# Performance work log

Measured on AMD Instinct MI355X. Metric: run time of the kernel, lower is better.

The kernel has to match this reference:

```python
import jax, jax.numpy as jnp
import numpy as np

NEG_INF = -9e15


def setup_inputs() -> dict:
    key = jax.random.key(0)
    k1, k2, k3, k4, k5, k6 = jax.random.split(key, 6)
    B, N, F_IN, F_OUT = 16, 2048, 256, 128
    inputs = jax.random.normal(k1, (B, N, F_IN), dtype=jnp.float32)
    adj_matrix = jax.random.randint(k2, (B, N, N), 0, 2, dtype=jnp.int32)
    W = jax.random.normal(k3, (F_OUT, F_IN), dtype=jnp.float32) * (1.0 / np.sqrt(F_IN))
    b_W = jax.random.normal(k4, (F_OUT,), dtype=jnp.float32) * 0.02
    a = jax.random.normal(k5, (1, 2 * F_OUT), dtype=jnp.float32) * (1.0 / np.sqrt(2 * F_OUT))
    b_a = jax.random.normal(k6, (1,), dtype=jnp.float32) * 0.02
    return {"inputs": inputs, "adj_matrix": adj_matrix, "W": W, "b_W": b_W, "a": a, "b_a": b_a}


def reference(inputs, adj_matrix, W, b_W, a, b_a):
    # wh: [B, N, H]
    wh = jnp.einsum('bnf,hf->bnh', inputs, W) + b_W
    H = wh.shape[-1]
    # linear_self_W([wh_i, wh_j]) = a1.wh_i + a2.wh_j + b  (rank-1 linear over concat)
    a1 = a[0, :H]
    a2 = a[0, H:]
    src = jnp.einsum('bnh,h->bn', wh, a1)  # [B, N] contribution of row node i
    dst = jnp.einsum('bnh,h->bn', wh, a2)  # [B, N] contribution of col node j
    e = jax.nn.leaky_relu(src[:, :, None] + dst[:, None, :] + b_a[0], negative_slope=0.01)
    e = jnp.where(adj_matrix > 0, e, NEG_INF)
    att = jax.nn.softmax(e, axis=-1)  # dropout in eval mode = identity
    return jax.nn.elu(jnp.einsum('bij,bjh->bih', att, wh))
```

## Files before the change

kernel.cpp:

```cpp
#include <hip/hip_runtime.h>


#define BDIM 16
#define NDIM 2048
#define FIN 256
#define HDIM 128

typedef short short8 __attribute__((ext_vector_type(8)));
typedef float floatx4 __attribute__((ext_vector_type(4)));

__device__ __forceinline__ unsigned short f2bf(float x) {
    unsigned int u = __float_as_uint(x);
    unsigned int r = (u + 0x7fffu + ((u >> 16) & 1u)) >> 16;
    return (unsigned short)r;
}
__device__ __forceinline__ float bf2f(unsigned short s) {
    return __uint_as_float(((unsigned int)s) << 16);
}

__global__ __launch_bounds__(256) void k_wh(const float* __restrict__ X,
                                            const float* __restrict__ W,
                                            const float* __restrict__ bW,
                                            const float* __restrict__ a,
                                            float* __restrict__ src,
                                            float* __restrict__ dst,
                                            unsigned short* __restrict__ whF) {
    __shared__ short lds[27648];
    short (*ah)[72] = (short(*)[72])lds;
    short (*al)[72] = (short(*)[72])(lds + 4608);
    short (*bh)[72] = (short(*)[72])(lds + 9216);
    short (*bl)[72] = (short(*)[72])(lds + 18432);
    short (*tb)[72] = (short(*)[72])lds;

    const int tid = threadIdx.x;
    const long row0 = (long)blockIdx.x * 64;
    const int w = tid >> 6, lane = tid & 63;
    const int lm = lane & 15, q = lane >> 4;

    float a1v[8], a2v[8], bwv[8];
    #pragma unroll
    for (int nt = 0; nt < 8; nt++) {
        a1v[nt] = a[nt * 16 + lm];
        a2v[nt] = a[HDIM + nt * 16 + lm];
        bwv[nt] = bW[nt * 16 + lm];
    }

    floatx4 acc[8];
    #pragma unroll
    for (int nt = 0; nt < 8; nt++) acc[nt] = (floatx4){0.f, 0.f, 0.f, 0.f};

    for (int k0 = 0; k0 < FIN; k0 += 64) {
        #pragma unroll
        for (int u = 0; u < 4; u++) {
            int idx = tid + u * 256;
            int r = idx >> 4, fc = (idx & 15) * 4;
            float4 v = *reinterpret_cast<const float4*>(X + (row0 + r) * FIN + k0 + fc);
            union { unsigned short s[4]; uint2 u2; } ph, pl;
            ph.s[0] = f2bf(v.x); pl.s[0] = f2bf(v.x - bf2f(ph.s[0]));
            ph.s[1] = f2bf(v.y); pl.s[1] = f2bf(v.y - bf2f(ph.s[1]));
            ph.s[2] = f2bf(v.z); pl.s[2] = f2bf(v.z - bf2f(ph.s[2]));
            ph.s[3] = f2bf(v.w); pl.s[3] = f2bf(v.w - bf2f(ph.s[3]));
            *reinterpret_cast<uint2*>(&ah[r][fc]) = ph.u2;
            *reinterpret_cast<uint2*>(&al[r][fc]) = pl.u2;
        }
        #pragma unroll
        for (int u = 0; u < 8; u++) {
            int idx = tid + u * 256;
            int hh = idx >> 4, fc = (idx & 15) * 4;
            float4 v = *reinterpret_cast<const float4*>(W + hh * FIN + k0 + fc);
            union { unsigned short s[4]; uint2 u2; } ph, pl;
            ph.s[0] = f2bf(v.x); pl.s[0] = f2bf(v.x - bf2f(ph.s[0]));
            ph.s[1] = f2bf(v.y); pl.s[1] = f2bf(v.y - bf2f(ph.s[1]));
            ph.s[2] = f2bf(v.z); pl.s[2] = f2bf(v.z - bf2f(ph.s[2]));
            ph.s[3] = f2bf(v.w); pl.s[3] = f2bf(v.w - bf2f(ph.s[3]));
            *reinterpret_cast<uint2*>(&bh[hh][fc]) = ph.u2;
            *reinterpret_cast<uint2*>(&bl[hh][fc]) = pl.u2;
        }
        __syncthreads();
        #pragma unroll
        for (int ks = 0; ks < 64; ks += 32) {
            short8 afh = *reinterpret_cast<const short8*>(&ah[w * 16 + lm][ks + q * 8]);
            short8 afl = *reinterpret_cast<const short8*>(&al[w * 16 + lm][ks + q * 8]);
            #pragma unroll
            for (int nt = 0; nt < 8; nt++) {
                short8 bfh = *reinterpret_cast<const short8*>(&bh[nt * 16 + lm][ks + q * 8]);
                short8 bfl = *reinterpret_cast<const short8*>(&bl[nt * 16 + lm][ks + q * 8]);
                acc[nt] = __builtin_amdgcn_mfma_f32_16x16x32_bf16(afh, bfh, acc[nt], 0, 0, 0);
                acc[nt] = __builtin_amdgcn_mfma_f32_16x16x32_bf16(afh, bfl, acc[nt], 0, 0, 0);
                acc[nt] = __builtin_amdgcn_mfma_f32_16x16x32_bf16(afl, bfh, acc[nt], 0, 0, 0);
            }
        }
        __syncthreads();
    }

    float s1[4] = {0.f, 0.f, 0.f, 0.f}, s2[4] = {0.f, 0.f, 0.f, 0.f};
    #pragma unroll
    for (int nt = 0; nt < 8; nt++) {
        #pragma unroll
        for (int r = 0; r < 4; r++) {
            float v = acc[nt][r] + bwv[nt];
            s1[r] += v * a1v[nt];
            s2[r] += v * a2v[nt];
            tb[nt * 16 + lm][w * 16 + q * 4 + r] = f2bf(v);
        }
    }
    #pragma unroll
    for (int r = 0; r < 4; r++) {
        #pragma unroll
        for (int o = 1; o < 16; o <<= 1) {
            s1[r] += __shfl_xor(s1[r], o);
            s2[r] += __shfl_xor(s2[r], o);
        }
    }
    if (lm == 0) {
        #pragma unroll
        for (int r = 0; r < 4; r++) {
            long row = row0 + w * 16 + q * 4 + r;
            src[row] = s1[r];
            dst[row] = s2[r];
        }
    }
    __syncthreads();
    const int b = (int)(row0 >> 11);
    const int jc0 = (int)((row0 & 2047) >> 5);
    const int f = tid >> 4;
    const int sub = tid & 15;
    const int jcrel = f >> 3, ht = f & 7;
    const size_t fbase = (((size_t)b * 64 + jc0 + jcrel) * 8 + ht) * 512;
    #pragma unroll
    for (int i = 0; i < 4; i++) {
        int l = sub * 4 + i;
        uint4 v = *reinterpret_cast<const uint4*>(&tb[ht * 16 + (l & 15)][jcrel * 32 + (l >> 4) * 8]);
        *reinterpret_cast<uint4*>(whF + fbase + l * 8) = v;
    }
}

__global__ __launch_bounds__(256) void k_attn(const int* __restrict__ adj,
                                              const unsigned short* __restrict__ whF,
                                              const float* __restrict__ src,
                                              const float* __restrict__ dst,
                                              const float* __restrict__ ba_p,
                                              float* __restrict__ out) {
    __shared__ float lred[64];
    __shared__ float linv_s[64];

    const int tid = threadIdx.x;
    const int b = blockIdx.x >> 5;
    const int i0 = (blockIdx.x & 31) * 64;
    const int wave = tid >> 6, lane = tid & 63;
    const int lm = lane & 15, q = lane >> 4;
    const int irow = i0 + wave * 16 + lm;

    const float si = src[b * NDIM + irow] + ba_p[0];
    const int* adjp = adj + ((size_t)(b * NDIM + irow)) * NDIM + q * 8;
    const float* dstp = dst + b * NDIM + q * 8;
    const unsigned short* whFb = whF + (size_t)b * 64 * 8 * 512 + lane * 8;

    floatx4 acc[8];
    #pragma unroll
    for (int hj = 0; hj < 8; hj++) acc[hj] = (floatx4){0.f, 0.f, 0.f, 0.f};
    float lpart = 0.f;

    int4 m[2][2];
    float4 d[2][2];
    short8 bfr[2][8];
    m[0][0] = *reinterpret_cast<const int4*>(adjp);
    m[0][1] = *reinterpret_cast<const int4*>(adjp + 4);
    d[0][0] = *reinterpret_cast<const float4*>(dstp);
    d[0][1] = *reinterpret_cast<const float4*>(dstp + 4);
    #pragma unroll
    for (int hj = 0; hj < 8; hj++) bfr[0][hj] = *reinterpret_cast<const short8*>(whFb + hj * 512);

    #pragma unroll 2
    for (int t = 0; t < NDIM / 32; t++) {
        const int p = t & 1, pn = p ^ 1;
        if (t + 1 < NDIM / 32) {
            const int* ap = adjp + (t + 1) * 32;
            m[pn][0] = *reinterpret_cast<const int4*>(ap);
            m[pn][1] = *reinterpret_cast<const int4*>(ap + 4);
            const float* dp = dstp + (t + 1) * 32;
            d[pn][0] = *reinterpret_cast<const float4*>(dp);
            d[pn][1] = *reinterpret_cast<const float4*>(dp + 4);
            const unsigned short* wp = whFb + (size_t)(t + 1) * 8 * 512;
            #pragma unroll
            for (int hj = 0; hj < 8; hj++)
                bfr[pn][hj] = *reinterpret_cast<const short8*>(wp + hj * 512);
        }
        const int* mi = reinterpret_cast<const int*>(&m[p][0]);
        const float* df = reinterpret_cast<const float*>(&d[p][0]);
        unsigned short wb[8];
        float ls = 0.f;
        #pragma unroll
        for (int j = 0; j < 8; j++) {
            float x = si + df[j];
            x = x > 0.f ? x : 0.01f * x;
            float wgt = mi[j] > 0 ? __expf(x) : 0.f;
            ls += wgt;
            wb[j] = f2bf(wgt);
        }
        lpart += ls;
        short8 af = *reinterpret_cast<const short8*>(wb);
        #pragma unroll
        for (int hj = 0; hj < 8; hj++)
            acc[hj] = __builtin_amdgcn_mfma_f32_16x16x32_bf16(af, bfr[p][hj], acc[hj], 0, 0, 0);
    }

    lpart += __shfl_xor(lpart, 16);
    lpart += __shfl_xor(lpart, 32);
    if (q == 0) lred[wave * 16 + lm] = lpart;
    __syncthreads();
    if (tid < 64) {
        float l = lred[tid];
        linv_s[tid] = l > 0.f ? 1.f / l : 0.f;
    }
    __syncthreads();

    #pragma unroll
    for (int r = 0; r < 4; r++) {
        int il = wave * 16 + q * 4 + r;
        float li = linv_s[il];
        size_t obase = ((size_t)(b * NDIM + i0 + il)) * HDIM + lm;
        #pragma unroll
        for (int hj = 0; hj < 8; hj++) {
            float x = acc[hj][r] * li;
            x = x > 0.f ? x : (__expf(x) - 1.f);
            out[obase + hj * 16] = x;
        }
    }
}

extern "C" void kernel_launch(void* const* d_in, const int* in_sizes, int n_in,
                              void* d_out, int out_size, void* d_ws, size_t ws_size,
                              hipStream_t stream) {
    const float* X  = (const float*)d_in[0];
    const int* adj  = (const int*)d_in[1];
    const float* W  = (const float*)d_in[2];
    const float* bW = (const float*)d_in[3];
    const float* a  = (const float*)d_in[4];
    const float* ba = (const float*)d_in[5];
    float* out = (float*)d_out;

    float* srcv = (float*)d_ws;
    float* dstv = srcv + BDIM * NDIM;
    unsigned short* whF = (unsigned short*)(dstv + BDIM * NDIM);

    k_wh<<<BDIM * NDIM / 64, 256, 0, stream>>>(X, W, bW, a, srcv, dstv, whF);
    k_attn<<<BDIM * (NDIM / 64), 256, 0, stream>>>(adj, whF, srcv, dstv, ba, out);
}
```

Measured before the change: 433.1 us.

## Deepen adjacency prefetch with nontemporal loads, remap blocks, and prescale logits for exp2

```diff
diff --git a/kernel.cpp b/kernel.cpp
--- a/kernel.cpp
+++ b/kernel.cpp
@@ -5,9 +5,11 @@
 #define NDIM 2048
 #define FIN 256
 #define HDIM 128
+#define LOG2E 1.4426950408889634f
 
 typedef short short8 __attribute__((ext_vector_type(8)));
 typedef float floatx4 __attribute__((ext_vector_type(4)));
+typedef int intx4 __attribute__((ext_vector_type(4)));
 
 __device__ __forceinline__ unsigned short f2bf(float x) {
     unsigned int u = __float_as_uint(x);
@@ -17,11 +19,15 @@
 __device__ __forceinline__ float bf2f(unsigned short s) {
     return __uint_as_float(((unsigned int)s) << 16);
 }
+__device__ __forceinline__ intx4 ldnt(const int* p) {
+    return __builtin_nontemporal_load(reinterpret_cast<const intx4*>(p));
+}
 
 __global__ __launch_bounds__(256) void k_wh(const float* __restrict__ X,
                                             const float* __restrict__ W,
                                             const float* __restrict__ bW,
                                             const float* __restrict__ a,
+                                            const float* __restrict__ ba_p,
                                             float* __restrict__ src,
                                             float* __restrict__ dst,
                                             unsigned short* __restrict__ whF) {
@@ -36,6 +42,7 @@
     const long row0 = (long)blockIdx.x * 64;
     const int w = tid >> 6, lane = tid & 63;
     const int lm = lane & 15, q = lane >> 4;
+    const float ba0 = ba_p[0];
 
     float a1v[8], a2v[8], bwv[8];
     #pragma unroll
@@ -116,8 +123,8 @@
         #pragma unroll
         for (int r = 0; r < 4; r++) {
             long row = row0 + w * 16 + q * 4 + r;
-            src[row] = s1[r];
-            dst[row] = s2[r];
+            src[row] = (s1[r] + ba0) * LOG2E;
+            dst[row] = s2[r] * LOG2E;
         }
     }
     __syncthreads();
@@ -139,19 +146,19 @@
                                               const unsigned short* __restrict__ whF,
                                               const float* __restrict__ src,
                                               const float* __restrict__ dst,
-                                              const float* __restrict__ ba_p,
                                               float* __restrict__ out) {
     __shared__ float lred[64];
     __shared__ float linv_s[64];
 
     const int tid = threadIdx.x;
-    const int b = blockIdx.x >> 5;
-    const int i0 = (blockIdx.x & 31) * 64;
+    const int bid = ((int)blockIdx.x & 7) * 64 + ((int)blockIdx.x >> 3);
+    const int b = bid >> 5;
+    const int i0 = (bid & 31) * 64;
     const int wave = tid >> 6, lane = tid & 63;
     const int lm = lane & 15, q = lane >> 4;
     const int irow = i0 + wave * 16 + lm;
 
-    const float si = src[b * NDIM + irow] + ba_p[0];
+    const float si = src[b * NDIM + irow];
     const int* adjp = adj + ((size_t)(b * NDIM + irow)) * NDIM + q * 8;
     const float* dstp = dst + b * NDIM + q * 8;
     const unsigned short* whFb = whF + (size_t)b * 64 * 8 * 512 + lane * 8;
@@ -161,40 +168,43 @@
     for (int hj = 0; hj < 8; hj++) acc[hj] = (floatx4){0.f, 0.f, 0.f, 0.f};
     float lpart = 0.f;
 
-    int4 m[2][2];
+    intx4 m[4][2];
     float4 d[2][2];
     short8 bfr[2][8];
-    m[0][0] = *reinterpret_cast<const int4*>(adjp);
-    m[0][1] = *reinterpret_cast<const int4*>(adjp + 4);
+    m[0][0] = ldnt(adjp);       m[0][1] = ldnt(adjp + 4);
+    m[1][0] = ldnt(adjp + 32);  m[1][1] = ldnt(adjp + 36);
+    m[2][0] = ldnt(adjp + 64);  m[2][1] = ldnt(adjp + 68);
     d[0][0] = *reinterpret_cast<const float4*>(dstp);
     d[0][1] = *reinterpret_cast<const float4*>(dstp + 4);
     #pragma unroll
     for (int hj = 0; hj < 8; hj++) bfr[0][hj] = *reinterpret_cast<const short8*>(whFb + hj * 512);
 
-    #pragma unroll 2
+    #pragma unroll 4
     for (int t = 0; t < NDIM / 32; t++) {
-        const int p = t & 1, pn = p ^ 1;
-        if (t + 1 < NDIM / 32) {
-            const int* ap = adjp + (t + 1) * 32;
-            m[pn][0] = *reinterpret_cast<const int4*>(ap);
-            m[pn][1] = *reinterpret_cast<const int4*>(ap + 4);
+        const int p = t & 3, pw = t & 1;
+        if (t < NDIM / 32 - 3) {
+            const int* ap = adjp + (t + 3) * 32;
+            m[(t + 3) & 3][0] = ldnt(ap);
+            m[(t + 3) & 3][1] = ldnt(ap + 4);
+        }
+        if (t < NDIM / 32 - 1) {
             const float* dp = dstp + (t + 1) * 32;
-            d[pn][0] = *reinterpret_cast<const float4*>(dp);
-            d[pn][1] = *reinterpret_cast<const float4*>(dp + 4);
+            d[pw ^ 1][0] = *reinterpret_cast<const float4*>(dp);
+            d[pw ^ 1][1] = *reinterpret_cast<const float4*>(dp + 4);
             const unsigned short* wp = whFb + (size_t)(t + 1) * 8 * 512;
             #pragma unroll
             for (int hj = 0; hj < 8; hj++)
-                bfr[pn][hj] = *reinterpret_cast<const short8*>(wp + hj * 512);
+                bfr[pw ^ 1][hj] = *reinterpret_cast<const short8*>(wp + hj * 512);
         }
         const int* mi = reinterpret_cast<const int*>(&m[p][0]);
-        const float* df = reinterpret_cast<const float*>(&d[p][0]);
+        const float* df = reinterpret_cast<const float*>(&d[pw][0]);
         unsigned short wb[8];
         float ls = 0.f;
         #pragma unroll
         for (int j = 0; j < 8; j++) {
             float x = si + df[j];
-            x = x > 0.f ? x : 0.01f * x;
-            float wgt = mi[j] > 0 ? __expf(x) : 0.f;
+            x = fmaxf(x, 0.01f * x);
+            float wgt = mi[j] > 0 ? __builtin_amdgcn_exp2f(x) : 0.f;
             ls += wgt;
             wb[j] = f2bf(wgt);
         }
@@ -202,7 +212,7 @@
         short8 af = *reinterpret_cast<const short8*>(wb);
         #pragma unroll
         for (int hj = 0; hj < 8; hj++)
-            acc[hj] = __builtin_amdgcn_mfma_f32_16x16x32_bf16(af, bfr[p][hj], acc[hj], 0, 0, 0);
+            acc[hj] = __builtin_amdgcn_mfma_f32_16x16x32_bf16(af, bfr[pw][hj], acc[hj], 0, 0, 0);
     }
 
     lpart += __shfl_xor(lpart, 16);
@@ -244,6 +254,6 @@
     float* dstv = srcv + BDIM * NDIM;
     unsigned short* whF = (unsigned short*)(dstv + BDIM * NDIM);
 
-    k_wh<<<BDIM * NDIM / 64, 256, 0, stream>>>(X, W, bW, a, srcv, dstv, whF);
-    k_attn<<<BDIM * (NDIM / 64), 256, 0, stream>>>(adj, whF, srcv, dstv, ba, out);
-}
+    k_wh<<<BDIM * NDIM / 64, 256, 0, stream>>>(X, W, bW, a, ba, srcv, dstv, whF);
+    k_attn<<<BDIM * (NDIM / 64), 256, 0, stream>>>(adj, whF, srcv, dstv, out);
+}
```

Result: slower. 812.5 us (+87.6%).
